# Optimization experiments

Hardware: AMD Instinct MI355X
Metric: run time of the kernel (lower is better)

## Reference

```python
import jax, jax.numpy as jnp
import numpy as np

N = 32768      # points (multiple of block_size)
D = 32         # h_dim (dim_per_head, also token feature dim)
H = 8          # num_heads
C = 3          # n_hashes
BS = 128       # block_size
R = 3          # coords_dim
K = 8          # num_w_per_dist
NB = N // BS   # buckets
EPS_LN = 1e-5


def _ln(x, w, b):
    mu = x.mean(-1, keepdims=True)
    var = ((x - mu) ** 2).mean(-1, keepdims=True)
    return (x - mu) * jax.lax.rsqrt(var + EPS_LN) * w + b


def setup_inputs() -> dict:
    key = jax.random.key(0)
    ks = jax.random.split(key, 16)
    s = 0.05
    return {
        "x": jax.random.normal(ks[0], (N, D), jnp.float32),
        "coords": jax.random.uniform(ks[1], (N, R), jnp.float32),
        "combined_shifts": jax.random.randint(ks[2], (C, H, N), 0, 2048),
        "norm1_w": jnp.ones((D,), jnp.float32),
        "norm1_b": jnp.zeros((D,), jnp.float32),
        "wq": s * jax.random.normal(ks[3], (D, H * D), jnp.float32),
        "wk": s * jax.random.normal(ks[4], (D, H * D), jnp.float32),
        "wv": s * jax.random.normal(ks[5], (D, H * D), jnp.float32),
        "w_rpe_w": s * jax.random.normal(ks[6], (H * D, R * K), jnp.float32),
        "alpha": jax.random.normal(ks[7], (H, D + R, C), jnp.float32),  # E2LSH (frozen)
        "out_w": s * jax.random.normal(ks[8], (H * D, D), jnp.float32),
        "out_b": jnp.zeros((D,), jnp.float32),
        "norm2_w": jnp.ones((D,), jnp.float32),
        "norm2_b": jnp.zeros((D,), jnp.float32),
        "ff1_w": s * jax.random.normal(ks[9], (D, D), jnp.float32),
        "ff1_b": jnp.zeros((D,), jnp.float32),
        "ff2_w": s * jax.random.normal(ks[10], (D, D), jnp.float32),
        "ff2_b": jnp.zeros((D,), jnp.float32),
    }


def _to_buckets(v, perm):
    # v: [H, N, d], perm: [C, H, N] -> [C, H, NB, BS, d]
    g = jnp.take_along_axis(v[None], perm[..., None], axis=2)
    return g.reshape(C, H, NB, BS, v.shape[-1])


def _from_buckets(s, inv):
    # s: [C, H, NB, BS, d], inv: [C, H, N] -> [C, H, N, d]
    f = s.reshape(C, H, N, s.shape[-1])
    return jnp.take_along_axis(f, inv[..., None], axis=2)


def _hept_forward(x, coords, combined_shifts, norm1_w, norm1_b, wq, wk, wv,
                  w_rpe_w, alpha, out_w, out_b, norm2_w, norm2_b,
                  ff1_w, ff1_b, ff2_w, ff2_b):
    xn = _ln(x, norm1_w, norm1_b)
    q = (xn @ wq).reshape(N, H, D)
    k = (xn @ wk).reshape(N, H, D)
    v = (xn @ wv).reshape(N, H, D)

    # prep_qk: RPE-derived kernel coordinates
    w = w_rpe_w.reshape(H, D, R, K)                       # (h d) (r k) -> h d r k
    qw = jnp.exp(jnp.minimum(w.sum(axis=1), 50.0)).sum(-1)  # [H, R]
    sqrt_w_r = jnp.sqrt(2.0 * qw)[None] * coords[:, None]    # [N, H, R]
    q_hat = jnp.concatenate([q, sqrt_w_r], axis=-1)          # [N, H, D+R]
    k_hat = jnp.concatenate([k, sqrt_w_r], axis=-1)

    q_hat = jnp.transpose(q_hat, (1, 0, 2))  # [H, N, D+R]
    k_hat = jnp.transpose(k_hat, (1, 0, 2))
    val = jnp.transpose(v, (1, 0, 2))        # [H, N, D]

    # LSH hashing (no-grad in original; outputs only feed integer argsort)
    qh = jax.lax.stop_gradient(jnp.einsum('hnd,hdc->chn', q_hat, alpha))
    kh = jax.lax.stop_gradient(jnp.einsum('hnd,hdc->chn', k_hat, alpha))
    hi = jnp.maximum(qh.max(-1, keepdims=True), kh.max(-1, keepdims=True))
    lo = jnp.minimum(qh.min(-1, keepdims=True), kh.min(-1, keepdims=True))
    hash_shift = hi - lo                                    # [C, H, 1]
    shift = combined_shifts.astype(qh.dtype) * hash_shift
    q_pos = jnp.argsort(qh + shift, axis=-1)                # [C, H, N]
    k_pos = jnp.argsort(kh + shift, axis=-1)

    s_query = _to_buckets(q_hat, q_pos)
    s_key = _to_buckets(k_hat, k_pos)
    s_value = _to_buckets(val, k_pos)

    # kernelized exponential attention within buckets
    q_sq = -0.5 * (s_query ** 2).sum(-1, keepdims=True)
    k_sq = -0.5 * (s_key ** 2).sum(-1, keepdims=True)
    dists = jnp.einsum('chbid,chbjd->chbij', s_query, s_key)
    qk = jnp.exp(jnp.minimum(dists + q_sq + jnp.swapaxes(k_sq, -1, -2), 0.0))
    denom = qk.sum(-1, keepdims=True) + 1e-20
    so = jnp.einsum('chbij,chbjd->chbid', qk, s_value)

    q_rev = jnp.argsort(q_pos, axis=-1)  # inverse permutation
    o = _from_buckets(so, q_rev).sum(0)        # [H, N, D]
    logits = _from_buckets(denom, q_rev).sum(0)  # [H, N, 1]
    out = o / logits

    out = jnp.transpose(out, (1, 0, 2)).reshape(N, H * D) @ out_w + out_b
    x = x + out  # dropout is identity in eval
    xn2 = _ln(x, norm2_w, norm2_b)
    ff = jax.nn.silu(xn2 @ ff1_w + ff1_b) @ ff2_w + ff2_b
    return x + ff


def reference(x, coords, combined_shifts, norm1_w, norm1_b, wq, wk, wv,
              w_rpe_w, alpha, out_w, out_b, norm2_w, norm2_b,
              ff1_w, ff1_b, ff2_w, ff2_b):
    return _hept_forward(x, coords, combined_shifts, norm1_w, norm1_b, wq, wk, wv,
                         w_rpe_w, alpha, out_w, out_b, norm2_w, norm2_b,
                         ff1_w, ff1_b, ff2_w, ff2_b)
```

## Files before the change

### kernel.cpp

```cpp
#include <hip/hip_runtime.h>

#define NPTS 32768
#define DIM 32
#define NH 8
#define NC 3
#define BSZ 128
#define NB 256
#define DH 35
#define DP 36
#define NSEG 24

typedef unsigned long long ull;
typedef __attribute__((ext_vector_type(8))) short bf16x8;
typedef __attribute__((ext_vector_type(4))) float f32x4;

__device__ __forceinline__ unsigned fmap(float f){
  unsigned b = __float_as_uint(f);
  return (b & 0x80000000u) ? ~b : (b | 0x80000000u);
}
__device__ __forceinline__ float funmap(unsigned u){
  unsigned b = (u & 0x80000000u) ? (u & 0x7fffffffu) : ~u;
  return __uint_as_float(b);
}
__device__ __forceinline__ unsigned short f2bf(float f){
  unsigned u = __float_as_uint(f);
  u += 0x7fffu + ((u >> 16) & 1u);
  return (unsigned short)(u >> 16);
}
__device__ __forceinline__ float bf2f(unsigned short h){
  return __uint_as_float(((unsigned)h) << 16);
}
__device__ __forceinline__ void cvt8(const float* f, bf16x8& hi, bf16x8& lo){
  #pragma unroll
  for (int j = 0; j < 8; ++j){
    unsigned short hb = f2bf(f[j]);
    hi[j] = (short)hb;
    lo[j] = (short)f2bf(f[j] - bf2f(hb));
  }
}

__device__ __forceinline__ void cswap(ull& a, ull& b, bool up){
  if ((a > b) == up){ ull t = a; a = b; b = t; }
}
__device__ __forceinline__ void bitonic8_initial(ull r[8], unsigned gbase){
  #pragma unroll
  for (int p = 0; p < 4; ++p){
    bool up = (((gbase + 2*p) & 2) == 0);
    cswap(r[2*p], r[2*p+1], up);
  }
  #pragma unroll
  for (int b = 0; b < 2; ++b){
    bool up = (((gbase + 4*b) & 4) == 0);
    cswap(r[4*b+0], r[4*b+2], up);
    cswap(r[4*b+1], r[4*b+3], up);
    cswap(r[4*b+0], r[4*b+1], up);
    cswap(r[4*b+2], r[4*b+3], up);
  }
  bool up = ((gbase & 8) == 0);
  #pragma unroll
  for (int i = 0; i < 4; ++i) cswap(r[i], r[i+4], up);
  #pragma unroll
  for (int b = 0; b < 2; ++b){
    cswap(r[4*b+0], r[4*b+2], up);
    cswap(r[4*b+1], r[4*b+3], up);
  }
  #pragma unroll
  for (int p = 0; p < 4; ++p) cswap(r[2*p], r[2*p+1], up);
}
__device__ __forceinline__ void bitonic8_finish(ull r[8], bool up){
  #pragma unroll
  for (int i = 0; i < 4; ++i) cswap(r[i], r[i+4], up);
  #pragma unroll
  for (int b = 0; b < 2; ++b){
    cswap(r[4*b+0], r[4*b+2], up);
    cswap(r[4*b+1], r[4*b+3], up);
  }
  #pragma unroll
  for (int p = 0; p < 4; ++p) cswap(r[2*p], r[2*p+1], up);
}

__global__ __launch_bounds__(256) void k_prep(const float* __restrict__ w_rpe,
        float* __restrict__ qw_sqrt, unsigned* __restrict__ slots_hi,
        unsigned* __restrict__ slots_lo){
  int tid = threadIdx.x;
  if (tid < NSEG){ slots_hi[tid] = 0u; slots_lo[tid] = 0xFFFFFFFFu; }
  __shared__ float S[24][8];
  if (tid < 192){
    int hr = tid >> 3, kk = tid & 7;
    int h = hr / 3, r = hr % 3;
    float s = 0.f;
    #pragma unroll
    for (int d = 0; d < DIM; ++d) s += w_rpe[(h*DIM + d)*24 + (r*8 + kk)];
    S[hr][kk] = expf(fminf(s, 50.f));
  }
  __syncthreads();
  if (tid < 24){
    float q = 0.f;
    #pragma unroll
    for (int kk = 0; kk < 8; ++kk) q += S[tid][kk];
    qw_sqrt[tid] = sqrtf(2.f * q);
  }
}

__global__ __launch_bounds__(256, 1) void k_qkv(const float* __restrict__ x,
        const float* __restrict__ n1w, const float* __restrict__ n1b,
        const float* __restrict__ coords, const float* __restrict__ wq,
        const float* __restrict__ wk, const float* __restrict__ wv,
        const float* __restrict__ qw_sqrt,
        float* __restrict__ q_hat, float* __restrict__ k_hat,
        float* __restrict__ val){
  __shared__ float W[3][DIM][NH*DIM];
  __shared__ float XT[128][33];
  int tid = threadIdx.x;
  for (int idx = tid; idx < 3*DIM*NH*DIM; idx += 256){
    int which = idx / (DIM*NH*DIM);
    int rem = idx % (DIM*NH*DIM);
    const float* src = which==0 ? wq : (which==1 ? wk : wv);
    W[which][rem/(NH*DIM)][rem%(NH*DIM)] = src[rem];
  }
  int base = blockIdx.x * 128;
  if (tid < 128){
    const float4* xr4 = (const float4*)(x + (size_t)(base + tid)*DIM);
    float4 v[8];
    float s = 0.f;
    #pragma unroll
    for (int u = 0; u < 8; ++u){ v[u] = xr4[u]; s += v[u].x+v[u].y+v[u].z+v[u].w; }
    float mu = s * (1.f/32.f);
    float var = 0.f;
    #pragma unroll
    for (int u = 0; u < 8; ++u){
      float a0=v[u].x-mu, a1=v[u].y-mu, a2=v[u].z-mu, a3=v[u].w-mu;
      var += a0*a0+a1*a1+a2*a2+a3*a3;
    }
    var *= (1.f/32.f);
    float rs = rsqrtf(var + 1e-5f);
    #pragma unroll
    for (int u = 0; u < 8; ++u){
      XT[tid][u*4+0] = (v[u].x-mu)*rs*n1w[u*4+0] + n1b[u*4+0];
      XT[tid][u*4+1] = (v[u].y-mu)*rs*n1w[u*4+1] + n1b[u*4+1];
      XT[tid][u*4+2] = (v[u].z-mu)*rs*n1w[u*4+2] + n1b[u*4+2];
      XT[tid][u*4+3] = (v[u].w-mu)*rs*n1w[u*4+3] + n1b[u*4+3];
    }
  }
  __syncthreads();
  int h = tid >> 5, i = tid & 31;
  float xr0[32], xr1[32], xr2[32], xr3[32];
  #pragma unroll
  for (int d = 0; d < 32; ++d){
    xr0[d] = XT[i][d]; xr1[d] = XT[i+32][d];
    xr2[d] = XT[i+64][d]; xr3[d] = XT[i+96][d];
  }
  float cp[4][3];
  #pragma unroll
  for (int rep = 0; rep < 4; ++rep)
    #pragma unroll
    for (int r = 0; r < 3; ++r)
      cp[rep][r] = qw_sqrt[h*3+r] * coords[(size_t)(base + i + 32*rep)*3 + r];

  #pragma unroll
  for (int which = 0; which < 3; ++which){
    for (int j0 = 0; j0 < 32; j0 += 4){
      float4 a0 = {0,0,0,0}, a1 = {0,0,0,0}, a2 = {0,0,0,0}, a3 = {0,0,0,0};
      #pragma unroll
      for (int d = 0; d < 32; ++d){
        float4 w4 = *(const float4*)&W[which][d][h*32 + j0];
        a0.x += xr0[d]*w4.x; a0.y += xr0[d]*w4.y; a0.z += xr0[d]*w4.z; a0.w += xr0[d]*w4.w;
        a1.x += xr1[d]*w4.x; a1.y += xr1[d]*w4.y; a1.z += xr1[d]*w4.z; a1.w += xr1[d]*w4.w;
        a2.x += xr2[d]*w4.x; a2.y += xr2[d]*w4.y; a2.z += xr2[d]*w4.z; a2.w += xr2[d]*w4.w;
        a3.x += xr3[d]*w4.x; a3.y += xr3[d]*w4.y; a3.z += xr3[d]*w4.z; a3.w += xr3[d]*w4.w;
      }
      #pragma unroll
      for (int rep = 0; rep < 4; ++rep){
        int n = base + i + 32*rep;
        float4 a = rep==0 ? a0 : (rep==1 ? a1 : (rep==2 ? a2 : a3));
        float* dst = which==0 ? (q_hat + ((size_t)h*NPTS + n)*DP)
                   : (which==1 ? (k_hat + ((size_t)h*NPTS + n)*DP)
                               : (val   + ((size_t)h*NPTS + n)*DIM));
        *(float4*)&dst[j0] = a;
      }
    }
  }
  #pragma unroll
  for (int rep = 0; rep < 4; ++rep){
    int n = base + i + 32*rep;
    float* dq = q_hat + ((size_t)h*NPTS + n)*DP;
    float* dk = k_hat + ((size_t)h*NPTS + n)*DP;
    dq[32]=cp[rep][0]; dq[33]=cp[rep][1]; dq[34]=cp[rep][2]; dq[35]=0.f;
    dk[32]=cp[rep][0]; dk[33]=cp[rep][1]; dk[34]=cp[rep][2]; dk[35]=0.f;
  }
}

__global__ __launch_bounds__(256) void k_hash(const float* __restrict__ q_hat,
        const float* __restrict__ k_hat, const float* __restrict__ alpha,
        float* __restrict__ qh_buf, float* __restrict__ kh_buf,
        unsigned* __restrict__ slots_hi, unsigned* __restrict__ slots_lo){
  int h = blockIdx.y;
  int n = blockIdx.x*256 + threadIdx.x;
  __shared__ float A[DH][NC];
  for (int idx = threadIdx.x; idx < DH*NC; idx += 256)
    A[idx/3][idx%3] = alpha[h*DH*NC + idx];
  __syncthreads();
  float qr[36], kr[36];
  const float4* qp = (const float4*)(q_hat + ((size_t)h*NPTS + n)*DP);
  const float4* kp = (const float4*)(k_hat + ((size_t)h*NPTS + n)*DP);
  #pragma unroll
  for (int u = 0; u < 9; ++u){
    *(float4*)&qr[u*4] = qp[u];
    *(float4*)&kr[u*4] = kp[u];
  }
  #pragma unroll
  for (int c = 0; c < NC; ++c){
    float qh = 0.f, kh = 0.f;
    #pragma unroll
    for (int d = 0; d < DH; ++d){ qh += qr[d]*A[d][c]; kh += kr[d]*A[d][c]; }
    qh_buf[((size_t)(c*NH + h))*NPTS + n] = qh;
    kh_buf[((size_t)(c*NH + h))*NPTS + n] = kh;
    float hi = fmaxf(qh, kh), lo = fminf(qh, kh);
    #pragma unroll
    for (int off = 32; off; off >>= 1){
      hi = fmaxf(hi, __shfl_xor(hi, off));
      lo = fminf(lo, __shfl_xor(lo, off));
    }
    if ((threadIdx.x & 63) == 0){
      atomicMax(&slots_hi[c*NH + h], fmap(hi));
      atomicMin(&slots_lo[c*NH + h], fmap(lo));
    }
  }
}

__global__ __launch_bounds__(1024) void k_sort_pack_local(
        const float* __restrict__ qh_buf, const float* __restrict__ kh_buf,
        const int* __restrict__ shifts,
        const unsigned* __restrict__ slots_hi, const unsigned* __restrict__ slots_lo,
        ull* __restrict__ packed){
  __shared__ ull ld[9216];
  int chunk = blockIdx.x;
  int lst = chunk >> 2;
  int seg = lst < NSEG ? lst : lst - NSEG;
  const float* buf = lst < NSEG ? qh_buf : kh_buf;
  unsigned coff = (unsigned)(chunk & 3) * 8192u;
  float hs = funmap(slots_hi[seg]) - funmap(slots_lo[seg]);
  unsigned tid = threadIdx.x;

  {
    ull r[8];
    unsigned gb = coff + 8u*tid;
    #pragma unroll
    for (int e = 0; e < 8; ++e){
      unsigned n = gb + e;
      size_t gi = (size_t)seg*NPTS + n;
      float key = buf[gi] + (float)shifts[gi] * hs;
      r[e] = ((ull)fmap(key) << 32) | n;
    }
    bitonic8_initial(r, gb);
    #pragma unroll
    for (int e = 0; e < 8; ++e) ld[9u*tid + e] = r[e];
  }
  __syncthreads();

  for (unsigned k = 16; k <= 8192u; k <<= 1){
    for (unsigned j = k >> 1; j >= 8; j >>= 1){
      #pragma unroll
      for (int it = 0; it < 4; ++it){
        unsigned p = tid + 1024u*it;
        unsigned i  = ((p & ~(j-1)) << 1) | (p & (j-1));
        unsigned x2 = i | j;
        bool up = (((coff + i) & k) == 0);
        unsigned pi = i + (i>>3), px = x2 + (x2>>3);
        ull a = ld[pi], b2 = ld[px];
        if ((a > b2) == up){ ld[pi] = b2; ld[px] = a; }
      }
      __syncthreads();
    }
    {
      ull r[8];
      #pragma unroll
      for (int e = 0; e < 8; ++e) r[e] = ld[9u*tid + e];
      bool up = (((coff + 8u*tid) & k) == 0);
      bitonic8_finish(r, up);
      #pragma unroll
      for (int e = 0; e < 8; ++e) ld[9u*tid + e] = r[e];
    }
    __syncthreads();
  }
  size_t base = (size_t)lst*NPTS + coff;
  for (unsigned idx = tid; idx < 8192; idx += 1024)
    packed[base + idx] = ld[idx + (idx>>3)];
}

__global__ __launch_bounds__(1024) void k_sort_local(ull* __restrict__ data,
        unsigned k_lo, unsigned k_hi){
  __shared__ ull ld[9216];
  int chunk = blockIdx.x;
  size_t base = (size_t)chunk * 8192;
  unsigned coff = (unsigned)(chunk & 3) * 8192u;
  unsigned tid = threadIdx.x;
  for (unsigned idx = tid; idx < 8192; idx += 1024)
    ld[idx + (idx>>3)] = data[base + idx];
  __syncthreads();
  for (unsigned k = k_lo; k <= k_hi; k <<= 1){
    unsigned j0 = (k >> 1) < 4096u ? (k >> 1) : 4096u;
    for (unsigned j = j0; j >= 8; j >>= 1){
      #pragma unroll
      for (int it = 0; it < 4; ++it){
        unsigned p = tid + 1024u*it;
        unsigned i  = ((p & ~(j-1)) << 1) | (p & (j-1));
        unsigned x2 = i | j;
        bool up = (((coff + i) & k) == 0);
        unsigned pi = i + (i>>3), px = x2 + (x2>>3);
        ull a = ld[pi], b2 = ld[px];
        if ((a > b2) == up){ ld[pi] = b2; ld[px] = a; }
      }
      __syncthreads();
    }
    {
      ull r[8];
      #pragma unroll
      for (int e = 0; e < 8; ++e) r[e] = ld[9u*tid + e];
      bool up = (((coff + 8u*tid) & k) == 0);
      bitonic8_finish(r, up);
      #pragma unroll
      for (int e = 0; e < 8; ++e) ld[9u*tid + e] = r[e];
    }
    __syncthreads();
  }
  for (unsigned idx = tid; idx < 8192; idx += 1024)
    data[base + idx] = ld[idx + (idx>>3)];
}

__global__ __launch_bounds__(256) void k_sort_global(ull* __restrict__ data,
        unsigned k, unsigned j){
  unsigned t = blockIdx.x*256 + threadIdx.x;
  unsigned seg = t >> 14;
  unsigned p = t & 16383u;
  unsigned i  = ((p & ~(j-1)) << 1) | (p & (j-1));
  unsigned x2 = i | j;
  size_t base = (size_t)seg << 15;
  bool up = ((i & k) == 0);
  ull a = data[base + i], b = data[base + x2];
  if ((a > b) == up){ data[base + i] = b; data[base + x2] = a; }
}

__global__ __launch_bounds__(512, 6) void k_attn(const float* __restrict__ q_hat,
        const float* __restrict__ k_hat, const float* __restrict__ val,
        const ull* __restrict__ packed, float* __restrict__ o_acc,
        float* __restrict__ logit_acc){
  __shared__ short KP[16384];
  __shared__ short Vt[4096];

  int t = threadIdx.x;
  int blk = blockIdx.x;
  int seg = blk >> 8;
  int b = blk & 255;
  int h = seg & 7;
  const ull* pq = packed + ((size_t)seg << 15) + (size_t)b*BSZ;
  const ull* pk = packed + ((size_t)(NSEG + seg) << 15) + (size_t)b*BSZ;

  int lane = t & 63;
  int w = t >> 6;
  int l15 = lane & 15, g = lane >> 4;
  int qrow = 16*w + l15;

  unsigned iqr = (unsigned)(pq[qrow] & 0xffffffffull);
  const float* qr = q_hat + ((size_t)h*NPTS + iqr)*DP;
  float4 qa = ((const float4*)qr)[2*g];
  float4 qb = ((const float4*)qr)[2*g+1];
  float4 qt = ((const float4*)qr)[8];

  {
    int r = t >> 2;
    int qd = t & 3;
    unsigned ik = (unsigned)(pk[r] & 0xffffffffull);
    const float* kr = k_hat + ((size_t)h*NPTS + ik)*DP;
    float fk[3] = {0.f, 0.f, 0.f};
    float vals[16];
    float psqk = 0.f;
    if (qd < 2){
      #pragma unroll
      for (int u = 0; u < 4; ++u)
        *(float4*)&vals[u*4] = ((const float4*)(kr + 16*qd))[u];
      #pragma unroll
      for (int d2 = 0; d2 < 16; ++d2) psqk += vals[d2]*vals[d2];
    } else if (qd == 2){
      float4 k4 = *(const float4*)(kr + 32);
      fk[0] = k4.x; fk[1] = k4.y; fk[2] = k4.z;
      psqk = k4.x*k4.x + k4.y*k4.y + k4.z*k4.z;
    }
    psqk += __shfl_xor(psqk, 1);
    psqk += __shfl_xor(psqk, 2);
    float ksq = -0.5f * psqk;
    if (qd == 2){
      vals[0]=fk[0]; vals[1]=fk[1]; vals[2]=fk[2];
      vals[3]=ksq; vals[4]=1.0f;
      #pragma unroll
      for (int d2 = 5; d2 < 16; ++d2) vals[d2] = 0.f;
    } else if (qd == 3){
      #pragma unroll
      for (int d2 = 0; d2 < 16; ++d2) vals[d2] = 0.f;
    }
    int rowbase = r*64;
    int sw = (r & 7) << 3;
    #pragma unroll
    for (int c0 = 0; c0 < 16; c0 += 4){
      int c = 16*qd + c0;
      unsigned short h0=f2bf(vals[c0]),   h1=f2bf(vals[c0+1]);
      unsigned short h2=f2bf(vals[c0+2]), h3=f2bf(vals[c0+3]);
      unsigned short l0=f2bf(vals[c0]  -bf2f(h0)), l1=f2bf(vals[c0+1]-bf2f(h1));
      unsigned short l2=f2bf(vals[c0+2]-bf2f(h2)), l3=f2bf(vals[c0+3]-bf2f(h3));
      int o = rowbase + (c ^ sw);
      uint2 hv, lv;
      hv.x = (unsigned)h0 | ((unsigned)h1 << 16);
      hv.y = (unsigned)h2 | ((unsigned)h3 << 16);
      lv.x = (unsigned)l0 | ((unsigned)l1 << 16);
      lv.y = (unsigned)l2 | ((unsigned)l3 << 16);
      *(uint2*)&KP[o] = hv;
      *(uint2*)&KP[8192 + o] = lv;
    }
    const float* vr = val + ((size_t)h*NPTS + ik)*DIM + 8*qd;
    float fv[8];
    *(float4*)&fv[0] = ((const float4*)vr)[0];
    *(float4*)&fv[4] = ((const float4*)vr)[1];
    #pragma unroll
    for (int d2 = 0; d2 < 8; ++d2){
      int vd = 8*qd + d2;
      Vt[vd*128 + (r ^ ((vd&7)<<3))] = (short)f2bf(fv[d2]);
    }
  }

  float f0[8] = {qa.x,qa.y,qa.z,qa.w, qb.x,qb.y,qb.z,qb.w};
  float psq = 0.f;
  #pragma unroll
  for (int j = 0; j < 8; ++j) psq += f0[j]*f0[j];
  if (g == 0) psq += qt.x*qt.x + qt.y*qt.y + qt.z*qt.z;
  psq += __shfl_xor(psq, 16);
  psq += __shfl_xor(psq, 32);
  float qsq = -0.5f * psq;
  bf16x8 qh0, ql0, qh1, ql1;
  cvt8(f0, qh0, ql0);
  float f1[8] = {0.f,0.f,0.f,0.f,0.f,0.f,0.f,0.f};
  if (g == 0){
    f1[0] = qt.x; f1[1] = qt.y; f1[2] = qt.z;
    f1[3] = 1.0f;
    f1[4] = qsq;
  }
  cvt8(f1, qh1, ql1);

  __syncthreads();

  f32x4 acc[8];
  #pragma unroll
  for (int kt = 0; kt < 8; ++kt) acc[kt] = (f32x4){0.f,0.f,0.f,0.f};
  #pragma unroll
  for (int kt = 0; kt < 8; ++kt){
    int krow = 16*kt + l15;
    int base = krow*64;
    int sw = (krow & 7) << 3;
    bf16x8 ah0 = *(const bf16x8*)&KP[base + ((8*g) ^ sw)];
    bf16x8 ah1 = *(const bf16x8*)&KP[base + ((32 + 8*g) ^ sw)];
    bf16x8 al0 = *(const bf16x8*)&KP[8192 + base + ((8*g) ^ sw)];
    bf16x8 al1 = *(const bf16x8*)&KP[8192 + base + ((32 + 8*g) ^ sw)];
    f32x4 c = acc[kt];
    c = __builtin_amdgcn_mfma_f32_16x16x32_bf16(ah0, qh0, c, 0, 0, 0);
    c = __builtin_amdgcn_mfma_f32_16x16x32_bf16(ah1, qh1, c, 0, 0, 0);
    c = __builtin_amdgcn_mfma_f32_16x16x32_bf16(al0, qh0, c, 0, 0, 0);
    c = __builtin_amdgcn_mfma_f32_16x16x32_bf16(al1, qh1, c, 0, 0, 0);
    c = __builtin_amdgcn_mfma_f32_16x16x32_bf16(ah0, ql0, c, 0, 0, 0);
    c = __builtin_amdgcn_mfma_f32_16x16x32_bf16(ah1, ql1, c, 0, 0, 0);
    acc[kt] = c;
  }

  __syncthreads();

  int qsw = (qrow & 7) << 3;
  float dena = 0.f;
  #pragma unroll
  for (int kt = 0; kt < 8; ++kt){
    f32x4 c = acc[kt];
    float p0 = __expf(fminf(c[0], 0.f));
    float p1 = __expf(fminf(c[1], 0.f));
    float p2 = __expf(fminf(c[2], 0.f));
    float p3 = __expf(fminf(c[3], 0.f));
    dena += p0 + p1 + p2 + p3;
    int key = 16*kt + 4*g;
    uint2 pv;
    pv.x = (unsigned)f2bf(p0) | ((unsigned)f2bf(p1) << 16);
    pv.y = (unsigned)f2bf(p2) | ((unsigned)f2bf(p3) << 16);
    *(uint2*)&KP[qrow*128 + (key ^ qsw)] = pv;
  }

  f32x4 oacc[2];
  oacc[0] = (f32x4){0.f,0.f,0.f,0.f};
  oacc[1] = (f32x4){0.f,0.f,0.f,0.f};
  #pragma unroll
  for (int ks = 0; ks < 4; ++ks){
    bf16x8 pA = *(const bf16x8*)&KP[qrow*128 + ((32*ks + 8*g) ^ qsw)];
    #pragma unroll
    for (int nt = 0; nt < 2; ++nt){
      int vd = 16*nt + l15;
      bf16x8 vB = *(const bf16x8*)&Vt[vd*128 + ((32*ks + 8*g) ^ ((vd&7)<<3))];
      oacc[nt] = __builtin_amdgcn_mfma_f32_16x16x32_bf16(pA, vB, oacc[nt], 0, 0, 0);
    }
  }

  {
    float d = dena;
    d += __shfl_xor(d, 16);
    d += __shfl_xor(d, 32);
    if (lane < 16) atomicAdd(&logit_acc[(size_t)h*NPTS + iqr], d + 1e-20f);
  }
  #pragma unroll
  for (int nt = 0; nt < 2; ++nt){
    f32x4 c = oacc[nt];
    #pragma unroll
    for (int r = 0; r < 4; ++r){
      unsigned iq = (unsigned)__shfl((int)iqr, 4*g + r);
      atomicAdd(&o_acc[((size_t)h*NPTS + iq)*DIM + 16*nt + l15], c[r]);
    }
  }
}

__global__ __launch_bounds__(256) void k_final(const float* __restrict__ x,
        const float* __restrict__ o_acc, const float* __restrict__ logit_acc,
        const float* __restrict__ out_w, const float* __restrict__ out_b,
        const float* __restrict__ n2w, const float* __restrict__ n2b,
        const float* __restrict__ f1w, const float* __restrict__ f1b,
        const float* __restrict__ f2w, const float* __restrict__ f2b,
        float* __restrict__ out){
  __shared__ float OW[256][32];
  __shared__ float F1[32][32];
  __shared__ float F2[32][32];
  int tid = threadIdx.x;
  for (int idx = tid; idx < 256*32; idx += 256) OW[idx/32][idx%32] = out_w[idx];
  for (int idx = tid; idx < 1024; idx += 256){
    F1[idx/32][idx%32] = f1w[idx];
    F2[idx/32][idx%32] = f2w[idx];
  }
  __syncthreads();
  int n = blockIdx.x*256 + tid;
  float attn[32];
  #pragma unroll
  for (int j = 0; j < 32; ++j) attn[j] = out_b[j];
  for (int h = 0; h < 8; ++h){
    float inv = 1.f / logit_acc[(size_t)h*NPTS + n];
    const float4* orow = (const float4*)(o_acc + ((size_t)h*NPTS + n)*DIM);
    #pragma unroll
    for (int u = 0; u < 8; ++u){
      float4 ov = orow[u];
      float vals[4] = {ov.x*inv, ov.y*inv, ov.z*inv, ov.w*inv};
      #pragma unroll
      for (int s = 0; s < 4; ++s){
        const float* wrow = &OW[h*32 + u*4 + s][0];
        #pragma unroll
        for (int j = 0; j < 32; ++j) attn[j] += vals[s] * wrow[j];
      }
    }
  }
  const float* xp = x + (size_t)n*DIM;
  float xr[32]; float s = 0.f;
  #pragma unroll
  for (int d = 0; d < 32; ++d){ xr[d] = xp[d] + attn[d]; s += xr[d]; }
  float mu = s * (1.f/32.f);
  float var = 0.f;
  #pragma unroll
  for (int d = 0; d < 32; ++d){ float dx = xr[d]-mu; var += dx*dx; }
  var *= (1.f/32.f);
  float rs = rsqrtf(var + 1e-5f);
  float xn2[32];
  #pragma unroll
  for (int d = 0; d < 32; ++d) xn2[d] = (xr[d]-mu)*rs*n2w[d] + n2b[d];
  float z[32];
  #pragma unroll
  for (int j = 0; j < 32; ++j) z[j] = f1b[j];
  #pragma unroll
  for (int d = 0; d < 32; ++d){
    float xd = xn2[d];
    const float* wrow = &F1[d][0];
    #pragma unroll
    for (int j = 0; j < 32; ++j) z[j] += xd * wrow[j];
  }
  #pragma unroll
  for (int j = 0; j < 32; ++j) z[j] = z[j] / (1.f + __expf(-z[j]));
  float y[32];
  #pragma unroll
  for (int d = 0; d < 32; ++d) y[d] = f2b[d];
  #pragma unroll
  for (int j = 0; j < 32; ++j){
    float zj = z[j];
    const float* wrow = &F2[j][0];
    #pragma unroll
    for (int d = 0; d < 32; ++d) y[d] += zj * wrow[d];
  }
  float* op = out + (size_t)n*DIM;
  #pragma unroll
  for (int d = 0; d < 32; ++d) op[d] = xr[d] + y[d];
}

extern "C" void kernel_launch(void* const* d_in, const int* in_sizes, int n_in,
                              void* d_out, int out_size, void* d_ws, size_t ws_size,
                              hipStream_t stream){
  const float* x      = (const float*)d_in[0];
  const float* coords = (const float*)d_in[1];
  const int*   shifts = (const int*)d_in[2];
  const float* n1w    = (const float*)d_in[3];
  const float* n1b    = (const float*)d_in[4];
  const float* wq     = (const float*)d_in[5];
  const float* wk     = (const float*)d_in[6];
  const float* wv     = (const float*)d_in[7];
  const float* w_rpe  = (const float*)d_in[8];
  const float* alpha  = (const float*)d_in[9];
  const float* out_w  = (const float*)d_in[10];
  const float* out_b  = (const float*)d_in[11];
  const float* n2w    = (const float*)d_in[12];
  const float* n2b    = (const float*)d_in[13];
  const float* f1w    = (const float*)d_in[14];
  const float* f1b    = (const float*)d_in[15];
  const float* f2w    = (const float*)d_in[16];
  const float* f2b    = (const float*)d_in[17];
  float* out = (float*)d_out;

  char* ws = (char*)d_ws;
  size_t off = 0;
  auto alloc = [&](size_t bytes){ size_t o = off; off += (bytes + 255) & ~(size_t)255; return o; };
  float*    qw_sqrt   = (float*)   (ws + alloc(24*4));
  unsigned* slots_hi  = (unsigned*)(ws + alloc(24*4));
  unsigned* slots_lo  = (unsigned*)(ws + alloc(24*4));
  float*    q_hat     = (float*)   (ws + alloc((size_t)NH*NPTS*DP*4));
  float*    k_hat     = (float*)   (ws + alloc((size_t)NH*NPTS*DP*4));
  float*    val       = (float*)   (ws + alloc((size_t)NH*NPTS*DIM*4));
  float*    qh_buf    = (float*)   (ws + alloc((size_t)NSEG*NPTS*4));
  float*    kh_buf    = (float*)   (ws + alloc((size_t)NSEG*NPTS*4));
  ull*      packed    = (ull*)     (ws + alloc((size_t)2*NSEG*NPTS*8));
  float*    o_acc     = (float*)   (ws + alloc((size_t)NH*NPTS*DIM*4));
  float*    logit_acc = (float*)   (ws + alloc((size_t)NH*NPTS*4));
  if (off > ws_size) return;

  hipMemsetAsync(o_acc, 0, (size_t)NH*NPTS*DIM*4, stream);
  hipMemsetAsync(logit_acc, 0, (size_t)NH*NPTS*4, stream);

  k_prep<<<1, 256, 0, stream>>>(w_rpe, qw_sqrt, slots_hi, slots_lo);
  k_qkv<<<NPTS/128, 256, 0, stream>>>(x, n1w, n1b, coords, wq, wk, wv, qw_sqrt,
                                      q_hat, k_hat, val);
  k_hash<<<dim3(NPTS/256, NH), 256, 0, stream>>>(q_hat, k_hat, alpha, qh_buf, kh_buf,
                                                 slots_hi, slots_lo);
  k_sort_pack_local<<<2*NSEG*4, 1024, 0, stream>>>(qh_buf, kh_buf, shifts,
                                                   slots_hi, slots_lo, packed);
  k_sort_global<<<(2*NSEG*16384)/256, 256, 0, stream>>>(packed, 16384u, 8192u);
  k_sort_local<<<2*NSEG*4, 1024, 0, stream>>>(packed, 16384u, 16384u);
  k_sort_global<<<(2*NSEG*16384)/256, 256, 0, stream>>>(packed, 32768u, 16384u);
  k_sort_global<<<(2*NSEG*16384)/256, 256, 0, stream>>>(packed, 32768u, 8192u);
  k_sort_local<<<2*NSEG*4, 1024, 0, stream>>>(packed, 32768u, 32768u);

  k_attn<<<NSEG*NB, 512, 0, stream>>>(q_hat, k_hat, val, packed, o_acc, logit_acc);
  k_final<<<NPTS/256, 256, 0, stream>>>(x, o_acc, logit_acc, out_w, out_b,
                                        n2w, n2b, f1w, f1b, f2w, f2b, out);
}
```

Baseline: 498.9 us.

## Fuse hashing into QKV, prepack bf16 hi/lo operands, merge sort passes

The E2LSH hash projection and min/max reduction move into the QKV kernel, so the separate hash kernel and its re-read of q/k disappear. Q and K are now stored once as pre-split bf16 hi/lo rows with the coordinate tail, squared-norm term and constant already packed, and V as bf16. The attention kernel then just copies these rows into LDS instead of converting per bucket, which cuts global traffic and ALU work in the hot kernel. Two global bitonic passes are merged into one 4-element kernel, and the probability packing uses the hardware v_cvt_pk_bf16_f32 instruction. The trade-off is a heavier QKV kernel with more register pressure and a higher occupancy bound requested for attention.

Result: faster. 460.4 us (-7.7%).

```diff
diff --git a/kernel.cpp b/kernel.cpp
--- a/kernel.cpp
+++ b/kernel.cpp
@@ -30,13 +30,10 @@
 __device__ __forceinline__ float bf2f(unsigned short h){
   return __uint_as_float(((unsigned)h) << 16);
 }
-__device__ __forceinline__ void cvt8(const float* f, bf16x8& hi, bf16x8& lo){
-  #pragma unroll
-  for (int j = 0; j < 8; ++j){
-    unsigned short hb = f2bf(f[j]);
-    hi[j] = (short)hb;
-    lo[j] = (short)f2bf(f[j] - bf2f(hb));
-  }
+__device__ __forceinline__ unsigned cvtpk_bf16(float a, float b){
+  unsigned r;
+  asm("v_cvt_pk_bf16_f32 %0, %1, %2" : "=v"(r) : "v"(a), "v"(b));
+  return r;
 }
 
 __device__ __forceinline__ void cswap(ull& a, ull& b, bool up){
@@ -106,11 +103,13 @@
         const float* __restrict__ n1w, const float* __restrict__ n1b,
         const float* __restrict__ coords, const float* __restrict__ wq,
         const float* __restrict__ wk, const float* __restrict__ wv,
-        const float* __restrict__ qw_sqrt,
-        float* __restrict__ q_hat, float* __restrict__ k_hat,
-        float* __restrict__ val){
+        const float* __restrict__ qw_sqrt, const float* __restrict__ alpha,
+        short* __restrict__ qpk, short* __restrict__ kpk, short* __restrict__ vbf,
+        float* __restrict__ qh_buf, float* __restrict__ kh_buf,
+        unsigned* __restrict__ slots_hi, unsigned* __restrict__ slots_lo){
   __shared__ float W[3][DIM][NH*DIM];
   __shared__ float XT[128][33];
+  __shared__ float AL[NH][DH][NC];
   int tid = threadIdx.x;
   for (int idx = tid; idx < 3*DIM*NH*DIM; idx += 256){
     int which = idx / (DIM*NH*DIM);
@@ -118,6 +117,8 @@
     const float* src = which==0 ? wq : (which==1 ? wk : wv);
     W[which][rem/(NH*DIM)][rem%(NH*DIM)] = src[rem];
   }
+  for (int idx = tid; idx < NH*DH*NC; idx += 256)
+    ((float*)AL)[idx] = alpha[idx];
   int base = blockIdx.x * 128;
   if (tid < 128){
     const float4* xr4 = (const float4*)(x + (size_t)(base + tid)*DIM);
@@ -150,80 +151,146 @@
     xr0[d] = XT[i][d]; xr1[d] = XT[i+32][d];
     xr2[d] = XT[i+64][d]; xr3[d] = XT[i+96][d];
   }
-  float cp[4][3];
-  #pragma unroll
-  for (int rep = 0; rep < 4; ++rep)
-    #pragma unroll
-    for (int r = 0; r < 3; ++r)
-      cp[rep][r] = qw_sqrt[h*3+r] * coords[(size_t)(base + i + 32*rep)*3 + r];
-
-  #pragma unroll
-  for (int which = 0; which < 3; ++which){
-    for (int j0 = 0; j0 < 32; j0 += 4){
-      float4 a0 = {0,0,0,0}, a1 = {0,0,0,0}, a2 = {0,0,0,0}, a3 = {0,0,0,0};
-      #pragma unroll
-      for (int d = 0; d < 32; ++d){
-        float4 w4 = *(const float4*)&W[which][d][h*32 + j0];
-        a0.x += xr0[d]*w4.x; a0.y += xr0[d]*w4.y; a0.z += xr0[d]*w4.z; a0.w += xr0[d]*w4.w;
-        a1.x += xr1[d]*w4.x; a1.y += xr1[d]*w4.y; a1.z += xr1[d]*w4.z; a1.w += xr1[d]*w4.w;
-        a2.x += xr2[d]*w4.x; a2.y += xr2[d]*w4.y; a2.z += xr2[d]*w4.z; a2.w += xr2[d]*w4.w;
-        a3.x += xr3[d]*w4.x; a3.y += xr3[d]*w4.y; a3.z += xr3[d]*w4.z; a3.w += xr3[d]*w4.w;
-      }
-      #pragma unroll
-      for (int rep = 0; rep < 4; ++rep){
-        int n = base + i + 32*rep;
-        float4 a = rep==0 ? a0 : (rep==1 ? a1 : (rep==2 ? a2 : a3));
-        float* dst = which==0 ? (q_hat + ((size_t)h*NPTS + n)*DP)
-                   : (which==1 ? (k_hat + ((size_t)h*NPTS + n)*DP)
-                               : (val   + ((size_t)h*NPTS + n)*DIM));
-        *(float4*)&dst[j0] = a;
-      }
-    }
-  }
-  #pragma unroll
-  for (int rep = 0; rep < 4; ++rep){
-    int n = base + i + 32*rep;
-    float* dq = q_hat + ((size_t)h*NPTS + n)*DP;
-    float* dk = k_hat + ((size_t)h*NPTS + n)*DP;
-    dq[32]=cp[rep][0]; dq[33]=cp[rep][1]; dq[34]=cp[rep][2]; dq[35]=0.f;
-    dk[32]=cp[rep][0]; dk[33]=cp[rep][1]; dk[34]=cp[rep][2]; dk[35]=0.f;
-  }
-}
-
-__global__ __launch_bounds__(256) void k_hash(const float* __restrict__ q_hat,
-        const float* __restrict__ k_hat, const float* __restrict__ alpha,
-        float* __restrict__ qh_buf, float* __restrict__ kh_buf,
-        unsigned* __restrict__ slots_hi, unsigned* __restrict__ slots_lo){
-  int h = blockIdx.y;
-  int n = blockIdx.x*256 + threadIdx.x;
-  __shared__ float A[DH][NC];
-  for (int idx = threadIdx.x; idx < DH*NC; idx += 256)
-    A[idx/3][idx%3] = alpha[h*DH*NC + idx];
-  __syncthreads();
-  float qr[36], kr[36];
-  const float4* qp = (const float4*)(q_hat + ((size_t)h*NPTS + n)*DP);
-  const float4* kp = (const float4*)(k_hat + ((size_t)h*NPTS + n)*DP);
-  #pragma unroll
-  for (int u = 0; u < 9; ++u){
-    *(float4*)&qr[u*4] = qp[u];
-    *(float4*)&kr[u*4] = kp[u];
-  }
-  #pragma unroll
-  for (int c = 0; c < NC; ++c){
-    float qh = 0.f, kh = 0.f;
-    #pragma unroll
-    for (int d = 0; d < DH; ++d){ qh += qr[d]*A[d][c]; kh += kr[d]*A[d][c]; }
-    qh_buf[((size_t)(c*NH + h))*NPTS + n] = qh;
-    kh_buf[((size_t)(c*NH + h))*NPTS + n] = kh;
-    float hi = fmaxf(qh, kh), lo = fminf(qh, kh);
-    #pragma unroll
-    for (int off = 32; off; off >>= 1){
-      hi = fmaxf(hi, __shfl_xor(hi, off));
-      lo = fminf(lo, __shfl_xor(lo, off));
-    }
-    if ((threadIdx.x & 63) == 0){
-      atomicMax(&slots_hi[c*NH + h], fmap(hi));
-      atomicMin(&slots_lo[c*NH + h], fmap(lo));
+  size_t nb = (size_t)h*NPTS + base + i;
+  short* qr0 = qpk + nb*96;      short* qr1 = qpk + (nb+32)*96;
+  short* qr2 = qpk + (nb+64)*96; short* qr3 = qpk + (nb+96)*96;
+  short* kr0 = kpk + nb*96;      short* kr1 = kpk + (nb+32)*96;
+  short* kr2 = kpk + (nb+64)*96; short* kr3 = kpk + (nb+96)*96;
+  short* vr0 = vbf + nb*32;      short* vr1 = vbf + (nb+32)*32;
+  short* vr2 = vbf + (nb+64)*32; short* vr3 = vbf + (nb+96)*32;
+
+  auto packrow = [&](short* row, int j0, float4 a){
+    unsigned short hx=f2bf(a.x), hy=f2bf(a.y), hz=f2bf(a.z), hw=f2bf(a.w);
+    uint2 hv, lv;
+    hv.x = (unsigned)hx | ((unsigned)hy << 16);
+    hv.y = (unsigned)hz | ((unsigned)hw << 16);
+    lv.x = (unsigned)f2bf(a.x - bf2f(hx)) | ((unsigned)f2bf(a.y - bf2f(hy)) << 16);
+    lv.y = (unsigned)f2bf(a.z - bf2f(hz)) | ((unsigned)f2bf(a.w - bf2f(hw)) << 16);
+    *(uint2*)&row[j0] = hv;
+    *(uint2*)&row[48 + j0] = lv;
+  };
+  auto packv = [&](short* row, int j0, float4 a){
+    uint2 hv;
+    hv.x = (unsigned)f2bf(a.x) | ((unsigned)f2bf(a.y) << 16);
+    hv.y = (unsigned)f2bf(a.z) | ((unsigned)f2bf(a.w) << 16);
+    *(uint2*)&row[j0] = hv;
+  };
+  auto hacc = [&](float4 a, int j0, float& sq, float (&hp)[3]){
+    sq += a.x*a.x; sq += a.y*a.y; sq += a.z*a.z; sq += a.w*a.w;
+    #pragma unroll
+    for (int c = 0; c < 3; ++c){
+      float t = hp[c];
+      t += a.x*AL[h][j0][c];   t += a.y*AL[h][j0+1][c];
+      t += a.z*AL[h][j0+2][c]; t += a.w*AL[h][j0+3][c];
+      hp[c] = t;
+    }
+  };
+
+  float qh_p0[3]={0,0,0}, qh_p1[3]={0,0,0}, qh_p2[3]={0,0,0}, qh_p3[3]={0,0,0};
+  float kh_p0[3]={0,0,0}, kh_p1[3]={0,0,0}, kh_p2[3]={0,0,0}, kh_p3[3]={0,0,0};
+  float qsq0=0.f,qsq1=0.f,qsq2=0.f,qsq3=0.f;
+  float ksq0=0.f,ksq1=0.f,ksq2=0.f,ksq3=0.f;
+
+  for (int j0 = 0; j0 < 32; j0 += 4){
+    float4 a0={0,0,0,0},a1={0,0,0,0},a2={0,0,0,0},a3={0,0,0,0};
+    #pragma unroll
+    for (int d = 0; d < 32; ++d){
+      float4 w4 = *(const float4*)&W[0][d][h*32 + j0];
+      a0.x += xr0[d]*w4.x; a0.y += xr0[d]*w4.y; a0.z += xr0[d]*w4.z; a0.w += xr0[d]*w4.w;
+      a1.x += xr1[d]*w4.x; a1.y += xr1[d]*w4.y; a1.z += xr1[d]*w4.z; a1.w += xr1[d]*w4.w;
+      a2.x += xr2[d]*w4.x; a2.y += xr2[d]*w4.y; a2.z += xr2[d]*w4.z; a2.w += xr2[d]*w4.w;
+      a3.x += xr3[d]*w4.x; a3.y += xr3[d]*w4.y; a3.z += xr3[d]*w4.z; a3.w += xr3[d]*w4.w;
+    }
+    hacc(a0, j0, qsq0, qh_p0); packrow(qr0, j0, a0);
+    hacc(a1, j0, qsq1, qh_p1); packrow(qr1, j0, a1);
+    hacc(a2, j0, qsq2, qh_p2); packrow(qr2, j0, a2);
+    hacc(a3, j0, qsq3, qh_p3); packrow(qr3, j0, a3);
+  }
+  for (int j0 = 0; j0 < 32; j0 += 4){
+    float4 a0={0,0,0,0},a1={0,0,0,0},a2={0,0,0,0},a3={0,0,0,0};
+    #pragma unroll
+    for (int d = 0; d < 32; ++d){
+      float4 w4 = *(const float4*)&W[1][d][h*32 + j0];
+      a0.x += xr0[d]*w4.x; a0.y += xr0[d]*w4.y; a0.z += xr0[d]*w4.z; a0.w += xr0[d]*w4.w;
+      a1.x += xr1[d]*w4.x; a1.y += xr1[d]*w4.y; a1.z += xr1[d]*w4.z; a1.w += xr1[d]*w4.w;
+      a2.x += xr2[d]*w4.x; a2.y += xr2[d]*w4.y; a2.z += xr2[d]*w4.z; a2.w += xr2[d]*w4.w;
+      a3.x += xr3[d]*w4.x; a3.y += xr3[d]*w4.y; a3.z += xr3[d]*w4.z; a3.w += xr3[d]*w4.w;
+    }
+    hacc(a0, j0, ksq0, kh_p0); packrow(kr0, j0, a0);
+    hacc(a1, j0, ksq1, kh_p1); packrow(kr1, j0, a1);
+    hacc(a2, j0, ksq2, kh_p2); packrow(kr2, j0, a2);
+    hacc(a3, j0, ksq3, kh_p3); packrow(kr3, j0, a3);
+  }
+  for (int j0 = 0; j0 < 32; j0 += 4){
+    float4 a0={0,0,0,0},a1={0,0,0,0},a2={0,0,0,0},a3={0,0,0,0};
+    #pragma unroll
+    for (int d = 0; d < 32; ++d){
+      float4 w4 = *(const float4*)&W[2][d][h*32 + j0];
+      a0.x += xr0[d]*w4.x; a0.y += xr0[d]*w4.y; a0.z += xr0[d]*w4.z; a0.w += xr0[d]*w4.w;
+      a1.x += xr1[d]*w4.x; a1.y += xr1[d]*w4.y; a1.z += xr1[d]*w4.z; a1.w += xr1[d]*w4.w;
+      a2.x += xr2[d]*w4.x; a2.y += xr2[d]*w4.y; a2.z += xr2[d]*w4.z; a2.w += xr2[d]*w4.w;
+      a3.x += xr3[d]*w4.x; a3.y += xr3[d]*w4.y; a3.z += xr3[d]*w4.z; a3.w += xr3[d]*w4.w;
+    }
+    packv(vr0, j0, a0); packv(vr1, j0, a1);
+    packv(vr2, j0, a2); packv(vr3, j0, a3);
+  }
+
+  auto writetail = [&](short* row, float c0, float c1, float c2, float x5, float x6){
+    unsigned short h0=f2bf(c0), h1=f2bf(c1), h2=f2bf(c2), h5=f2bf(x5), h6=f2bf(x6);
+    uint4 hv, lv, zz;
+    zz.x = 0; zz.y = 0; zz.z = 0; zz.w = 0;
+    hv.x = (unsigned)h0 | ((unsigned)h1 << 16);
+    hv.y = (unsigned)h2 | ((unsigned)h5 << 16);
+    hv.z = (unsigned)h6; hv.w = 0;
+    lv.x = (unsigned)f2bf(c0 - bf2f(h0)) | ((unsigned)f2bf(c1 - bf2f(h1)) << 16);
+    lv.y = (unsigned)f2bf(c2 - bf2f(h2)) | ((unsigned)f2bf(x5 - bf2f(h5)) << 16);
+    lv.z = (unsigned)f2bf(x6 - bf2f(h6)); lv.w = 0;
+    *(uint4*)&row[32] = hv;
+    *(uint4*)&row[40] = zz;
+    *(uint4*)&row[80] = lv;
+    *(uint4*)&row[88] = zz;
+  };
+
+  float mx[3] = {-3.4e38f, -3.4e38f, -3.4e38f};
+  float mn[3] = { 3.4e38f,  3.4e38f,  3.4e38f};
+  auto fin = [&](int n, short* qrow, short* krow, float qsqp, float ksqp,
+                 const float (&qhp)[3], const float (&khp)[3]){
+    float c0 = qw_sqrt[h*3+0] * coords[(size_t)n*3+0];
+    float c1 = qw_sqrt[h*3+1] * coords[(size_t)n*3+1];
+    float c2 = qw_sqrt[h*3+2] * coords[(size_t)n*3+2];
+    float csq = c0*c0 + c1*c1 + c2*c2;
+    float qsq = -0.5f*(qsqp + csq);
+    float ksq = -0.5f*(ksqp + csq);
+    writetail(qrow, c0, c1, c2, 1.0f, qsq);
+    writetail(krow, c0, c1, c2, ksq, 1.0f);
+    #pragma unroll
+    for (int c = 0; c < 3; ++c){
+      float qh = qhp[c];
+      qh += c0*AL[h][32][c]; qh += c1*AL[h][33][c]; qh += c2*AL[h][34][c];
+      float kh = khp[c];
+      kh += c0*AL[h][32][c]; kh += c1*AL[h][33][c]; kh += c2*AL[h][34][c];
+      qh_buf[(size_t)(c*NH + h)*NPTS + n] = qh;
+      kh_buf[(size_t)(c*NH + h)*NPTS + n] = kh;
+      mx[c] = fmaxf(mx[c], fmaxf(qh, kh));
+      mn[c] = fminf(mn[c], fminf(qh, kh));
+    }
+  };
+  fin(base + i,      qr0, kr0, qsq0, ksq0, qh_p0, kh_p0);
+  fin(base + i + 32, qr1, kr1, qsq1, ksq1, qh_p1, kh_p1);
+  fin(base + i + 64, qr2, kr2, qsq2, ksq2, qh_p2, kh_p2);
+  fin(base + i + 96, qr3, kr3, qsq3, ksq3, qh_p3, kh_p3);
+
+  #pragma unroll
+  for (int c = 0; c < 3; ++c){
+    float mx_ = mx[c], mn_ = mn[c];
+    #pragma unroll
+    for (int off = 1; off <= 16; off <<= 1){
+      mx_ = fmaxf(mx_, __shfl_xor(mx_, off));
+      mn_ = fminf(mn_, __shfl_xor(mn_, off));
+    }
+    if ((tid & 31) == 0){
+      atomicMax(&slots_hi[c*NH + h], fmap(mx_));
+      atomicMin(&slots_lo[c*NH + h], fmap(mn_));
     }
   }
 }
@@ -341,8 +408,20 @@
   if ((a > b) == up){ data[base + i] = b; data[base + x2] = a; }
 }
 
-__global__ __launch_bounds__(512, 6) void k_attn(const float* __restrict__ q_hat,
-        const float* __restrict__ k_hat, const float* __restrict__ val,
+__global__ __launch_bounds__(256) void k_sort_global2(ull* __restrict__ data){
+  unsigned t = blockIdx.x*256 + threadIdx.x;
+  unsigned seg = t >> 13;
+  unsigned i = t & 8191u;
+  size_t base = ((size_t)seg << 15) + i;
+  ull e0 = data[base], e1 = data[base + 8192], e2 = data[base + 16384], e3 = data[base + 24576];
+  cswap(e0, e2, true); cswap(e1, e3, true);
+  cswap(e0, e1, true); cswap(e2, e3, true);
+  data[base] = e0; data[base + 8192] = e1;
+  data[base + 16384] = e2; data[base + 24576] = e3;
+}
+
+__global__ __launch_bounds__(512, 8) void k_attn(const short* __restrict__ qpk,
+        const short* __restrict__ kpk, const short* __restrict__ vbf,
         const ull* __restrict__ packed, float* __restrict__ o_acc,
         float* __restrict__ logit_acc){
   __shared__ short KP[16384];
@@ -362,89 +441,47 @@
   int qrow = 16*w + l15;
 
   unsigned iqr = (unsigned)(pq[qrow] & 0xffffffffull);
-  const float* qr = q_hat + ((size_t)h*NPTS + iqr)*DP;
-  float4 qa = ((const float4*)qr)[2*g];
-  float4 qb = ((const float4*)qr)[2*g+1];
-  float4 qt = ((const float4*)qr)[8];
+  const short* qrp = qpk + ((size_t)h*NPTS + iqr)*96;
+  bf16x8 qh0 = *(const bf16x8*)&qrp[8*g];
+  bf16x8 ql0 = *(const bf16x8*)&qrp[48 + 8*g];
+  bf16x8 qh1 = (bf16x8){0,0,0,0,0,0,0,0};
+  bf16x8 ql1 = (bf16x8){0,0,0,0,0,0,0,0};
+  if (g < 2){
+    qh1 = *(const bf16x8*)&qrp[32 + 8*g];
+    ql1 = *(const bf16x8*)&qrp[80 + 8*g];
+  }
 
   {
     int r = t >> 2;
     int qd = t & 3;
     unsigned ik = (unsigned)(pk[r] & 0xffffffffull);
-    const float* kr = k_hat + ((size_t)h*NPTS + ik)*DP;
-    float fk[3] = {0.f, 0.f, 0.f};
-    float vals[16];
-    float psqk = 0.f;
-    if (qd < 2){
-      #pragma unroll
-      for (int u = 0; u < 4; ++u)
-        *(float4*)&vals[u*4] = ((const float4*)(kr + 16*qd))[u];
-      #pragma unroll
-      for (int d2 = 0; d2 < 16; ++d2) psqk += vals[d2]*vals[d2];
-    } else if (qd == 2){
-      float4 k4 = *(const float4*)(kr + 32);
-      fk[0] = k4.x; fk[1] = k4.y; fk[2] = k4.z;
-      psqk = k4.x*k4.x + k4.y*k4.y + k4.z*k4.z;
-    }
-    psqk += __shfl_xor(psqk, 1);
-    psqk += __shfl_xor(psqk, 2);
-    float ksq = -0.5f * psqk;
-    if (qd == 2){
-      vals[0]=fk[0]; vals[1]=fk[1]; vals[2]=fk[2];
-      vals[3]=ksq; vals[4]=1.0f;
-      #pragma unroll
-      for (int d2 = 5; d2 < 16; ++d2) vals[d2] = 0.f;
-    } else if (qd == 3){
-      #pragma unroll
-      for (int d2 = 0; d2 < 16; ++d2) vals[d2] = 0.f;
-    }
     int rowbase = r*64;
     int sw = (r & 7) << 3;
-    #pragma unroll
-    for (int c0 = 0; c0 < 16; c0 += 4){
-      int c = 16*qd + c0;
-      unsigned short h0=f2bf(vals[c0]),   h1=f2bf(vals[c0+1]);
-      unsigned short h2=f2bf(vals[c0+2]), h3=f2bf(vals[c0+3]);
-      unsigned short l0=f2bf(vals[c0]  -bf2f(h0)), l1=f2bf(vals[c0+1]-bf2f(h1));
-      unsigned short l2=f2bf(vals[c0+2]-bf2f(h2)), l3=f2bf(vals[c0+3]-bf2f(h3));
-      int o = rowbase + (c ^ sw);
-      uint2 hv, lv;
-      hv.x = (unsigned)h0 | ((unsigned)h1 << 16);
-      hv.y = (unsigned)h2 | ((unsigned)h3 << 16);
-      lv.x = (unsigned)l0 | ((unsigned)l1 << 16);
-      lv.y = (unsigned)l2 | ((unsigned)l3 << 16);
-      *(uint2*)&KP[o] = hv;
-      *(uint2*)&KP[8192 + o] = lv;
-    }
-    const float* vr = val + ((size_t)h*NPTS + ik)*DIM + 8*qd;
-    float fv[8];
-    *(float4*)&fv[0] = ((const float4*)vr)[0];
-    *(float4*)&fv[4] = ((const float4*)vr)[1];
+    const short* krp = kpk + ((size_t)h*NPTS + ik)*96;
+    if (qd < 3){
+      bf16x8 h0 = *(const bf16x8*)&krp[16*qd];
+      bf16x8 h1 = *(const bf16x8*)&krp[16*qd + 8];
+      bf16x8 l0 = *(const bf16x8*)&krp[48 + 16*qd];
+      bf16x8 l1 = *(const bf16x8*)&krp[56 + 16*qd];
+      *(bf16x8*)&KP[rowbase + ((16*qd) ^ sw)] = h0;
+      *(bf16x8*)&KP[rowbase + ((16*qd + 8) ^ sw)] = h1;
+      *(bf16x8*)&KP[8192 + rowbase + ((16*qd) ^ sw)] = l0;
+      *(bf16x8*)&KP[8192 + rowbase + ((16*qd + 8) ^ sw)] = l1;
+    } else {
+      bf16x8 z = (bf16x8){0,0,0,0,0,0,0,0};
+      *(bf16x8*)&KP[rowbase + (48 ^ sw)] = z;
+      *(bf16x8*)&KP[rowbase + (56 ^ sw)] = z;
+      *(bf16x8*)&KP[8192 + rowbase + (48 ^ sw)] = z;
+      *(bf16x8*)&KP[8192 + rowbase + (56 ^ sw)] = z;
+    }
+    const short* vrp = vbf + ((size_t)h*NPTS + ik)*32 + 8*qd;
+    bf16x8 vv = *(const bf16x8*)vrp;
     #pragma unroll
     for (int d2 = 0; d2 < 8; ++d2){
       int vd = 8*qd + d2;
-      Vt[vd*128 + (r ^ ((vd&7)<<3))] = (short)f2bf(fv[d2]);
-    }
-  }
-
-  float f0[8] = {qa.x,qa.y,qa.z,qa.w, qb.x,qb.y,qb.z,qb.w};
-  float psq = 0.f;
-  #pragma unroll
-  for (int j = 0; j < 8; ++j) psq += f0[j]*f0[j];
-  if (g == 0) psq += qt.x*qt.x + qt.y*qt.y + qt.z*qt.z;
-  psq += __shfl_xor(psq, 16);
-  psq += __shfl_xor(psq, 32);
-  float qsq = -0.5f * psq;
-  bf16x8 qh0, ql0, qh1, ql1;
-  cvt8(f0, qh0, ql0);
-  float f1[8] = {0.f,0.f,0.f,0.f,0.f,0.f,0.f,0.f};
-  if (g == 0){
-    f1[0] = qt.x; f1[1] = qt.y; f1[2] = qt.z;
-    f1[3] = 1.0f;
-    f1[4] = qsq;
-  }
-  cvt8(f1, qh1, ql1);
-
+      Vt[vd*128 + (r ^ ((vd & 7) << 3))] = vv[d2];
+    }
+  }
   __syncthreads();
 
   f32x4 acc[8];
@@ -483,8 +520,8 @@
     dena += p0 + p1 + p2 + p3;
     int key = 16*kt + 4*g;
     uint2 pv;
-    pv.x = (unsigned)f2bf(p0) | ((unsigned)f2bf(p1) << 16);
-    pv.y = (unsigned)f2bf(p2) | ((unsigned)f2bf(p3) << 16);
+    pv.x = cvtpk_bf16(p0, p1);
+    pv.y = cvtpk_bf16(p2, p3);
     *(uint2*)&KP[qrow*128 + (key ^ qsw)] = pv;
   }
 
@@ -624,9 +661,9 @@
   float*    qw_sqrt   = (float*)   (ws + alloc(24*4));
   unsigned* slots_hi  = (unsigned*)(ws + alloc(24*4));
   unsigned* slots_lo  = (unsigned*)(ws + alloc(24*4));
-  float*    q_hat     = (float*)   (ws + alloc((size_t)NH*NPTS*DP*4));
-  float*    k_hat     = (float*)   (ws + alloc((size_t)NH*NPTS*DP*4));
-  float*    val       = (float*)   (ws + alloc((size_t)NH*NPTS*DIM*4));
+  short*    qpk       = (short*)   (ws + alloc((size_t)NH*NPTS*96*2));
+  short*    kpk       = (short*)   (ws + alloc((size_t)NH*NPTS*96*2));
+  short*    vbf       = (short*)   (ws + alloc((size_t)NH*NPTS*32*2));
   float*    qh_buf    = (float*)   (ws + alloc((size_t)NSEG*NPTS*4));
   float*    kh_buf    = (float*)   (ws + alloc((size_t)NSEG*NPTS*4));
   ull*      packed    = (ull*)     (ws + alloc((size_t)2*NSEG*NPTS*8));
@@ -639,18 +676,16 @@
 
   k_prep<<<1, 256, 0, stream>>>(w_rpe, qw_sqrt, slots_hi, slots_lo);
   k_qkv<<<NPTS/128, 256, 0, stream>>>(x, n1w, n1b, coords, wq, wk, wv, qw_sqrt,
-                                      q_hat, k_hat, val);
-  k_hash<<<dim3(NPTS/256, NH), 256, 0, stream>>>(q_hat, k_hat, alpha, qh_buf, kh_buf,
-                                                 slots_hi, slots_lo);
+                                      alpha, qpk, kpk, vbf, qh_buf, kh_buf,
+                                      slots_hi, slots_lo);
   k_sort_pack_local<<<2*NSEG*4, 1024, 0, stream>>>(qh_buf, kh_buf, shifts,
                                                    slots_hi, slots_lo, packed);
   k_sort_global<<<(2*NSEG*16384)/256, 256, 0, stream>>>(packed, 16384u, 8192u);
   k_sort_local<<<2*NSEG*4, 1024, 0, stream>>>(packed, 16384u, 16384u);
-  k_sort_global<<<(2*NSEG*16384)/256, 256, 0, stream>>>(packed, 32768u, 16384u);
-  k_sort_global<<<(2*NSEG*16384)/256, 256, 0, stream>>>(packed, 32768u, 8192u);
+  k_sort_global2<<<(2*NSEG*8192)/256, 256, 0, stream>>>(packed);
   k_sort_local<<<2*NSEG*4, 1024, 0, stream>>>(packed, 32768u, 32768u);
 
-  k_attn<<<NSEG*NB, 512, 0, stream>>>(q_hat, k_hat, val, packed, o_acc, logit_acc);
+  k_attn<<<NSEG*NB, 512, 0, stream>>>(qpk, kpk, vbf, packed, o_acc, logit_acc);
   k_final<<<NPTS/256, 256, 0, stream>>>(x, o_acc, logit_acc, out_w, out_b,
                                         n2w, n2b, f1w, f1b, f2w, f2b, out);
 }
```
